# Kernel tuning notes

Measured on AMD Instinct MI355X. Metric: run time of the kernel, lower is better.

The kernel has to match this reference:

```python
import jax, jax.numpy as jnp
import numpy as np

GRID = (128, 128, 16)
VSIZE = 0.5  # voxel_size, pc_range = 0
B, V, N, K, C = 2, 100000, 8192, 8, 64
EPS = 1e-5
OFFSETS = [(dx, dy, dz) for dx in (-1, 0, 1) for dy in (-1, 0, 1) for dz in (-1, 0, 1)]


def setup_inputs() -> dict:
    key = jax.random.key(0)
    ks = jax.random.split(key, 8)
    world = jnp.array([GRID[0] * VSIZE, GRID[1] * VSIZE, GRID[2] * VSIZE], jnp.float32)
    keypoints = jax.random.uniform(ks[0], (B, N, K, 3), jnp.float32) * world
    query_feature = jax.random.normal(ks[1], (B, N, C), jnp.float32)
    voxel_feature = jax.random.normal(ks[2], (B, V, C), jnp.float32)
    # unique voxel coords per batch (hash-map / sparse-tensor semantics)
    cells = GRID[0] * GRID[1] * GRID[2]
    perm = jax.vmap(lambda k: jax.random.permutation(k, cells)[:V])(jax.random.split(ks[3], B))
    x = perm // (GRID[1] * GRID[2])
    rem = perm % (GRID[1] * GRID[2])
    voxel_coords = jnp.stack([x, rem // GRID[2], rem % GRID[2]], -1).astype(jnp.int32)
    W1 = jax.random.normal(ks[4], (27, C, C), jnp.float32) * 0.05
    W2 = jax.random.normal(ks[5], (27, C, C), jnp.float32) * 0.05
    proj_W = jax.random.normal(ks[6], (C, C), jnp.float32) / np.sqrt(C).astype(np.float32)
    proj_b = jnp.zeros((C,), jnp.float32)
    return dict(keypoints=keypoints, query_feature=query_feature,
                voxel_feature=voxel_feature, voxel_coords=voxel_coords,
                W1=W1, bn1_gamma=jnp.ones((C,), jnp.float32), bn1_beta=jnp.zeros((C,), jnp.float32),
                W2=W2, bn2_gamma=jnp.ones((C,), jnp.float32), bn2_beta=jnp.zeros((C,), jnp.float32),
                proj_W=proj_W, proj_b=proj_b)


def _subm_conv(feats, grid, cb, cxyz, W):
    # feats: (M, C); grid: (B, X, Y, Z) int32 flat row index or -1; W: (27, Cin, Cout)
    out = jnp.zeros((feats.shape[0], W.shape[-1]), feats.dtype)
    for k, (dx, dy, dz) in enumerate(OFFSETS):
        nx, ny, nz = cxyz[:, 0] + dx, cxyz[:, 1] + dy, cxyz[:, 2] + dz
        valid = (nx >= 0) & (nx < GRID[0]) & (ny >= 0) & (ny < GRID[1]) & (nz >= 0) & (nz < GRID[2])
        nidx = grid[cb, jnp.clip(nx, 0, GRID[0] - 1), jnp.clip(ny, 0, GRID[1] - 1), jnp.clip(nz, 0, GRID[2] - 1)]
        nidx = jnp.where(valid, nidx, -1)
        nf = jnp.where((nidx >= 0)[:, None], feats[jnp.maximum(nidx, 0)], jnp.zeros((), feats.dtype))
        out = out + nf @ W[k]
    return out


def _bn_relu(x, gamma, beta):
    # BatchNorm1d in training mode: batch stats (biased var), then ReLU
    mu = x.mean(0)
    var = jnp.var(x, axis=0)
    return jax.nn.relu((x - mu) * jax.lax.rsqrt(var + EPS) * gamma + beta)


def reference(keypoints, query_feature, voxel_feature, voxel_coords,
              W1, bn1_gamma, bn1_beta, W2, bn2_gamma, bn2_beta, proj_W, proj_b):
    coords = voxel_coords.reshape(-1, 3).astype(jnp.int32)
    cb = jnp.repeat(jnp.arange(B, dtype=jnp.int32), V)
    # dense grid hash: cell -> flat voxel row, -1 if empty (replaces Python dict)
    grid = jnp.full((B,) + GRID, -1, jnp.int32)
    grid = grid.at[cb, coords[:, 0], coords[:, 1], coords[:, 2]].set(jnp.arange(B * V, dtype=jnp.int32))
    feats = voxel_feature.reshape(-1, C)
    feats = _bn_relu(_subm_conv(feats, grid, cb, coords, W1), bn1_gamma, bn1_beta)
    feats = _bn_relu(_subm_conv(feats, grid, cb, coords, W2), bn2_gamma, bn2_beta)
    # quantize keypoints (pc_range = 0, trunc == floor since coords >= 0)
    q = (keypoints / VSIZE).astype(jnp.int32)
    q = jnp.clip(q, 0, jnp.array(GRID, jnp.int32) - 1)  # (B, N, K, 3)
    bidx = jnp.arange(B, dtype=jnp.int32)[:, None, None]
    idx = grid[bidx, q[..., 0], q[..., 1], q[..., 2]]   # (B, N, K); -1 -> fallback row 0
    sampled = feats[jnp.maximum(idx, 0)]                 # (B, N, K, C)
    fused = (sampled.mean(2) + query_feature) @ proj_W.T + proj_b
    voxel_indices = jnp.concatenate(
        [jnp.broadcast_to(bidx[..., None], (B, N, K, 1)), q], axis=-1).reshape(-1, 4)
    return fused, voxel_indices
```

## Files before the change

### kernel.cpp

```cpp
#include <hip/hip_runtime.h>
#include <hip/hip_bf16.h>
#include <math.h>

#define GX 128
#define GY 128
#define GZ 16
#define CELLS (GX*GY*GZ)
#define NCELLT (NB*CELLS)
#define NB 2
#define NV 100000
#define NM (NB*NV)
#define NN 8192
#define NK 8
#define NC 64
#define EPSV 1e-5f
#define TM 256
#define NTILE 98
#define NBLK (8*NTILE)
#define NMT (NBLK*TM)
#define KPH 7

typedef __attribute__((ext_vector_type(8))) short short8;
typedef __attribute__((ext_vector_type(4))) float floatx4;

__device__ __forceinline__ float bf2f(unsigned short u) {
    unsigned int x = ((unsigned int)u) << 16;
    return __builtin_bit_cast(float, x);
}
__device__ __forceinline__ unsigned short f2bf(float f) {
    unsigned int u = __builtin_bit_cast(unsigned int, f);
    return (unsigned short)((u + 0x7fffu + ((u >> 16) & 1u)) >> 16);
}

__global__ void k_init(int* __restrict__ grid, float* __restrict__ stats,
                       unsigned short* __restrict__ featA) {
    int i = blockIdx.x * 256 + threadIdx.x;
    if (i < NCELLT) grid[i] = -1;
    else if (i < NCELLT + 512) stats[i - NCELLT] = 0.f;
    else if (i < NCELLT + 512 + 64) featA[(size_t)NM * 64 + (i - NCELLT - 512)] = 0;
}

__global__ void k_scatter(const int* __restrict__ coords, int* __restrict__ grid) {
    int gid = blockIdx.x * 256 + threadIdx.x;
    if (gid >= NM) return;
    int b = (gid >= NV) ? 1 : 0;
    int x = coords[gid * 3 + 0];
    int y = coords[gid * 3 + 1];
    int z = coords[gid * 3 + 2];
    grid[((b * GX + x) * GY + y) * GZ + z] = gid;
}

__global__ void k_count(const int* __restrict__ grid, int* __restrict__ bcnt) {
    __shared__ int wt[4];
    int t = threadIdx.x;
    int occ = (grid[blockIdx.x * 256 + t] >= 0) ? 1 : 0;
    int w = t >> 6;
    unsigned long long m = __ballot(occ);
    if ((t & 63) == 0) wt[w] = __popcll(m);
    __syncthreads();
    if (t == 0) bcnt[blockIdx.x] = wt[0] + wt[1] + wt[2] + wt[3];
}

__global__ void k_scan2048(const int* __restrict__ bcnt, int* __restrict__ boff) {
    __shared__ int s[256];
    int t = threadIdx.x;
    int v[8], sum = 0;
    #pragma unroll
    for (int j = 0; j < 8; ++j) {
        int x = bcnt[t * 8 + j];
        v[j] = sum;
        sum += x;
    }
    s[t] = sum;
    __syncthreads();
    for (int off = 1; off < 256; off <<= 1) {
        int x = (t >= off) ? s[t - off] : 0;
        __syncthreads();
        s[t] += x;
        __syncthreads();
    }
    int excl = s[t] - sum;
    #pragma unroll
    for (int j = 0; j < 8; ++j) boff[t * 8 + j] = excl + v[j];
}

__global__ void k_assign(const int* __restrict__ gold, const int* __restrict__ boff,
                         int* __restrict__ gnew, int* __restrict__ perm,
                         int* __restrict__ scell) {
    __shared__ int wt[4];
    int t = threadIdx.x;
    int cell = blockIdx.x * 256 + t;
    int old = gold[cell];
    int occ = (old >= 0) ? 1 : 0;
    int w = t >> 6, lane = t & 63;
    unsigned long long m = __ballot(occ);
    int lp = __popcll(m & ((1ULL << lane) - 1ULL));
    if (lane == 63) wt[w] = lp + occ;
    __syncthreads();
    int wbase = 0;
    #pragma unroll
    for (int j = 0; j < 4; ++j) if (j < w) wbase += wt[j];
    int nid = boff[blockIdx.x] + wbase + lp;
    if (occ) {
        gnew[cell] = nid;
        perm[nid] = old;
        scell[nid] = cell;
    } else {
        gnew[cell] = -1;
    }
}

__global__ void k_fb(const int* __restrict__ vcoords, const int* __restrict__ gnew,
                     int* __restrict__ fbp) {
    if (threadIdx.x == 0 && blockIdx.x == 0) {
        int cell = (vcoords[0] * GY + vcoords[1]) * GZ + vcoords[2];
        fbp[0] = gnew[cell];
    }
}

__global__ void k_nbr(const int* __restrict__ scell, const int* __restrict__ gnew,
                      int* __restrict__ nid) {
    int m = blockIdx.x * 256 + threadIdx.x;
    if (m >= NMT) return;
    int cell = (m < NM) ? scell[m] : -1;
    int x = 0, y = 0, z = 0;
    if (cell >= 0) { x = (cell >> 11) & 127; y = (cell >> 4) & 127; z = cell & 15; }
    #pragma unroll
    for (int k = 0; k < 28; ++k) {
        int ni = NM;
        if (k < 27 && cell >= 0) {
            int dx = k / 9 - 1, dy = (k / 3) % 3 - 1, dz = k % 3 - 1;
            int nx = x + dx, ny = y + dy, nz = z + dz;
            if (nx >= 0 && nx < GX && ny >= 0 && ny < GY && nz >= 0 && nz < GZ) {
                int g = gnew[cell + dx * (GY * GZ) + dy * GZ + dz];
                ni = (g < 0) ? NM : g;
            }
        }
        nid[(size_t)k * NMT + m] = ni;
    }
}

__global__ void k_wprep(const float* __restrict__ W1, const float* __restrict__ W2,
                        unsigned short* __restrict__ Wt1, unsigned short* __restrict__ Wt2) {
    int e = blockIdx.x * 256 + threadIdx.x;
    if (e >= 28 * 512) return;
    int lane = e & 63;
    int fr = (e >> 6) & 7;
    int k = e >> 9;
    int ct = fr >> 1, ks = fr & 1;
    int quad = lane >> 4, n16 = lane & 15;
    int co = ct * 16 + n16;
    #pragma unroll
    for (int j = 0; j < 8; ++j) {
        int ci = ks * 32 + quad * 8 + j;
        unsigned short w1 = 0, w2 = 0;
        if (k < 27) {
            w1 = f2bf(W1[(k << 12) + ci * 64 + co]);
            w2 = f2bf(W2[(k << 12) + ci * 64 + co]);
        }
        Wt1[(size_t)e * 8 + j] = w1;
        Wt2[(size_t)e * 8 + j] = w2;
    }
}

__global__ void k_tobf16s(const float* __restrict__ in, const int* __restrict__ perm,
                          unsigned short* __restrict__ out) {
    int i = blockIdx.x * 256 + threadIdx.x;
    if (i >= NM * 8) return;
    int mrow = i >> 3, part = i & 7;
    int src = perm[mrow];
    const float4* s = (const float4*)(in + (size_t)src * 64 + part * 8);
    float4 a = s[0], b = s[1];
    ushort4 lo, hi;
    lo.x = f2bf(a.x); lo.y = f2bf(a.y); lo.z = f2bf(a.z); lo.w = f2bf(a.w);
    hi.x = f2bf(b.x); hi.y = f2bf(b.y); hi.z = f2bf(b.z); hi.w = f2bf(b.w);
    ushort4* d = (ushort4*)(out + (size_t)mrow * 64 + part * 8);
    d[0] = lo; d[1] = hi;
}

__global__ __launch_bounds__(256, 2) void k_conv(
    const unsigned short* __restrict__ feats, const int* __restrict__ nid,
    const unsigned short* __restrict__ Wt,
    unsigned short* __restrict__ out, float* __restrict__ gsum, float* __restrict__ gsq)
{
    __shared__ unsigned short s_b[KPH * 4096];

    int tid = threadIdx.x;
    int bid = blockIdx.x;
    int tile = (bid & 7) * NTILE + (bid >> 3);
    int m0 = tile * TM;

    int w = tid >> 6, lane = tid & 63;
    int quad = lane >> 4, n16 = lane & 15;
    const unsigned short* fq = feats + quad * 8;
    const int* nbase = nid + m0 + w * 64 + n16;

    short8 afr[3][8];

    auto issueA = [&](const int* nr, short8* af) {
        #pragma unroll
        for (int rt = 0; rt < 4; ++rt) {
            const unsigned short* r0 = fq + (size_t)nr[rt] * 64;
            af[rt * 2 + 0] = *(const short8*)(r0);
            af[rt * 2 + 1] = *(const short8*)(r0 + 32);
        }
    };

    floatx4 acc[4][4];
    #pragma unroll
    for (int rt = 0; rt < 4; ++rt)
        #pragma unroll
        for (int ct = 0; ct < 4; ++ct)
            acc[rt][ct] = (floatx4){0.f, 0.f, 0.f, 0.f};

    const uint4* wt4 = (const uint4*)Wt;

    for (int ph = 0; ph < 4; ++ph) {
        int k0 = ph * KPH;
        __syncthreads();

        uint4 breg[KPH * 2];
        #pragma unroll
        for (int i = 0; i < KPH * 2; ++i)
            breg[i] = wt4[(size_t)k0 * 512 + i * 256 + tid];

        int nidr[KPH][4];
        #pragma unroll
        for (int j = 0; j < KPH; ++j)
            #pragma unroll
            for (int rt = 0; rt < 4; ++rt)
                nidr[j][rt] = nbase[(size_t)(k0 + j) * NMT + rt * 16];

        #pragma unroll
        for (int i = 0; i < KPH * 2; ++i)
            ((uint4*)s_b)[i * 256 + tid] = breg[i];

        issueA(nidr[0], afr[0]);
        issueA(nidr[1], afr[1]);
        __syncthreads();

        #pragma unroll
        for (int j = 0; j < KPH; ++j) {
            if (j + 2 < KPH) issueA(nidr[j + 2], afr[(j + 2) % 3]);
            __builtin_amdgcn_sched_barrier(0);

            const unsigned short* bb = s_b + j * 4096;
            short8 bfr[8];
            #pragma unroll
            for (int fr = 0; fr < 8; ++fr)
                bfr[fr] = *(const short8*)(bb + fr * 512 + lane * 8);

            const short8* ac = afr[j % 3];
            #pragma unroll
            for (int ks = 0; ks < 2; ++ks)
                #pragma unroll
                for (int rt = 0; rt < 4; ++rt)
                    #pragma unroll
                    for (int ct = 0; ct < 4; ++ct)
                        acc[rt][ct] = __builtin_amdgcn_mfma_f32_16x16x32_bf16(
                            ac[rt * 2 + ks], bfr[ct * 2 + ks], acc[rt][ct], 0, 0, 0);
            __builtin_amdgcn_sched_barrier(0);
        }
    }

    #pragma unroll
    for (int rt = 0; rt < 4; ++rt) {
        int rbase = m0 + w * 64 + rt * 16 + quad * 4;
        #pragma unroll
        for (int rg = 0; rg < 4; ++rg) {
            int m = rbase + rg;
            if (m < NM) {
                #pragma unroll
                for (int ct = 0; ct < 4; ++ct)
                    out[(size_t)m * 64 + ct * 16 + n16] = f2bf(acc[rt][ct][rg]);
            }
        }
    }

    float ps[4], pq[4];
    #pragma unroll
    for (int ct = 0; ct < 4; ++ct) { ps[ct] = 0.f; pq[ct] = 0.f; }
    #pragma unroll
    for (int rt = 0; rt < 4; ++rt)
        #pragma unroll
        for (int ct = 0; ct < 4; ++ct)
            #pragma unroll
            for (int rg = 0; rg < 4; ++rg) {
                float v = acc[rt][ct][rg];
                ps[ct] += v;
                pq[ct] += v * v;
            }
    #pragma unroll
    for (int ct = 0; ct < 4; ++ct) {
        ps[ct] += __shfl_xor(ps[ct], 16);
        ps[ct] += __shfl_xor(ps[ct], 32);
        pq[ct] += __shfl_xor(pq[ct], 16);
        pq[ct] += __shfl_xor(pq[ct], 32);
    }
    __syncthreads();
    float* red = (float*)s_b;
    if (lane < 16) {
        #pragma unroll
        for (int ct = 0; ct < 4; ++ct) {
            red[w * 64 + ct * 16 + n16]       = ps[ct];
            red[256 + w * 64 + ct * 16 + n16] = pq[ct];
        }
    }
    __syncthreads();
    if (tid < 64) {
        float ts = 0.f, tq = 0.f;
        #pragma unroll
        for (int ww = 0; ww < 4; ++ww) {
            ts += red[ww * 64 + tid];
            tq += red[256 + ww * 64 + tid];
        }
        atomicAdd(gsum + tid, ts);
        atomicAdd(gsq + tid, tq);
    }
}

__global__ void k_bncoef(const float* __restrict__ gsum, const float* __restrict__ gsq,
                         const float* __restrict__ gamma, const float* __restrict__ beta,
                         float* __restrict__ coef) {
    int c = threadIdx.x;
    if (c >= 64) return;
    float mu = gsum[c] / (float)NM;
    float var = gsq[c] / (float)NM - mu * mu;
    float scale = gamma[c] / sqrtf(var + EPSV);
    coef[c] = scale;
    coef[64 + c] = beta[c] - mu * scale;
}

__global__ void k_bnapply(const unsigned short* __restrict__ in, const float* __restrict__ coef,
                          unsigned short* __restrict__ out) {
    int i = blockIdx.x * 256 + threadIdx.x;
    if (i >= NM * 8) return;
    int c8 = (i & 7) * 8;
    uint4 v = ((const uint4*)in)[i];
    unsigned int vv[4] = {v.x, v.y, v.z, v.w};
    unsigned int oo[4];
    #pragma unroll
    for (int j = 0; j < 4; ++j) {
        int c = c8 + j * 2;
        float lo = bf2f((unsigned short)(vv[j] & 0xffffu));
        float hi = bf2f((unsigned short)(vv[j] >> 16));
        lo = fmaxf(lo * coef[c]     + coef[64 + c],     0.f);
        hi = fmaxf(hi * coef[c + 1] + coef[64 + c + 1], 0.f);
        oo[j] = (unsigned int)f2bf(lo) | ((unsigned int)f2bf(hi) << 16);
    }
    uint4 o = {oo[0], oo[1], oo[2], oo[3]};
    ((uint4*)out)[i] = o;
}

__global__ __launch_bounds__(256) void k_sample(
    const float* __restrict__ kp, const float* __restrict__ query,
    const unsigned short* __restrict__ conv2, const float* __restrict__ coef2,
    const int* __restrict__ grid, const int* __restrict__ fbp,
    const float* __restrict__ projW, const float* __restrict__ projB,
    float* __restrict__ out_fused, float* __restrict__ out_vi)
{
    __shared__ float s_pw[64 * 65];
    __shared__ float s_mean[4][64];
    __shared__ int   s_idx[4][8];

    int tid = threadIdx.x;
    for (int e = tid; e < 4096; e += 256) {
        int co = e >> 6, c = e & 63;
        s_pw[co * 65 + c] = projW[e];
    }

    int w = tid >> 6, lane = tid & 63;
    int row = blockIdx.x * 4 + w;
    int b = row >> 13;
    float sc = coef2[lane];
    float sh = coef2[64 + lane];
    int fb = fbp[0];
    __syncthreads();

    if (lane < 8) {
        int kk = lane;
        const float* kpp = kp + ((size_t)row * 8 + kk) * 3;
        int qx = min(max((int)(kpp[0] * 2.0f), 0), GX - 1);
        int qy = min(max((int)(kpp[1] * 2.0f), 0), GY - 1);
        int qz = min(max((int)(kpp[2] * 2.0f), 0), GZ - 1);
        s_idx[w][kk] = grid[((b * GX + qx) * GY + qy) * GZ + qz];
        float4 vi = make_float4((float)b, (float)qx, (float)qy, (float)qz);
        *(float4*)(out_vi + ((size_t)row * 8 + kk) * 4) = vi;
    }
    __syncthreads();

    float acc = 0.f;
    #pragma unroll
    for (int kk = 0; kk < 8; ++kk) {
        int gi = s_idx[w][kk];
        gi = gi < 0 ? fb : gi;
        float v = bf2f(conv2[(size_t)gi * 64 + lane]);
        acc += fmaxf(v * sc + sh, 0.f);
    }
    float mean = acc * 0.125f + query[(size_t)row * 64 + lane];
    s_mean[w][lane] = mean;
    __syncthreads();

    float f = projB[lane];
    const float* pwr = s_pw + lane * 65;
    const float* mv = s_mean[w];
    #pragma unroll 8
    for (int c = 0; c < 64; ++c) f += mv[c] * pwr[c];
    out_fused[(size_t)row * 64 + lane] = f;
}

extern "C" void kernel_launch(void* const* d_in, const int* in_sizes, int n_in,
                              void* d_out, int out_size, void* d_ws, size_t ws_size,
                              hipStream_t stream) {
    const float* keypoints = (const float*)d_in[0];
    const float* query     = (const float*)d_in[1];
    const float* vfeat     = (const float*)d_in[2];
    const int*   vcoords   = (const int*)d_in[3];
    const float* W1        = (const float*)d_in[4];
    const float* g1        = (const float*)d_in[5];
    const float* b1        = (const float*)d_in[6];
    const float* W2        = (const float*)d_in[7];
    const float* g2        = (const float*)d_in[8];
    const float* b2        = (const float*)d_in[9];
    const float* pW        = (const float*)d_in[10];
    const float* pb        = (const float*)d_in[11];

    char* ws = (char*)d_ws;
    int*            gold  = (int*)ws;
    int*            gnew  = (int*)(ws + 2097152);
    float*          stats = (float*)(ws + 4194304);
    int*            fbp   = (int*)(ws + 4196352);
    int*            bcnt  = (int*)(ws + 4196608);
    int*            boff  = (int*)(ws + 4204800);
    int*            perm  = (int*)(ws + 4212992);
    int*            scell = (int*)(ws + 5012992);
    unsigned short* Wt1   = (unsigned short*)(ws + 5812992);
    unsigned short* Wt2   = (unsigned short*)(ws + 6042368);
    unsigned short* featA = (unsigned short*)(ws + 6271744);
    int*            nidt  = (int*)(ws + 31872000);
    unsigned short* convo = (unsigned short*)(ws + 54350848);

    float* sum1 = stats,       *sq1 = stats + 64,  *coef1 = stats + 128;
    float* sum2 = stats + 256, *sq2 = stats + 320, *coef2 = stats + 384;

    int initN = NCELLT + 512 + 64;
    k_init<<<(initN + 255) / 256, 256, 0, stream>>>(gold, stats, featA);
    k_scatter<<<(NM + 255) / 256, 256, 0, stream>>>(vcoords, gold);

    k_count<<<NCELLT / 256, 256, 0, stream>>>(gold, bcnt);
    k_scan2048<<<1, 256, 0, stream>>>(bcnt, boff);
    k_assign<<<NCELLT / 256, 256, 0, stream>>>(gold, boff, gnew, perm, scell);
    k_fb<<<1, 64, 0, stream>>>(vcoords, gnew, fbp);
    k_nbr<<<NMT / 256, 256, 0, stream>>>(scell, gnew, nidt);

    k_wprep<<<(28 * 512 + 255) / 256, 256, 0, stream>>>(W1, W2, Wt1, Wt2);
    k_tobf16s<<<(NM * 8 + 255) / 256, 256, 0, stream>>>(vfeat, perm, featA);

    k_conv<<<NBLK, 256, 0, stream>>>(featA, nidt, Wt1, convo, sum1, sq1);
    k_bncoef<<<1, 64, 0, stream>>>(sum1, sq1, g1, b1, coef1);
    k_bnapply<<<(NM * 8 + 255) / 256, 256, 0, stream>>>(convo, coef1, featA);

    k_conv<<<NBLK, 256, 0, stream>>>(featA, nidt, Wt2, convo, sum2, sq2);
    k_bncoef<<<1, 64, 0, stream>>>(sum2, sq2, g2, b2, coef2);

    float* out_fused = (float*)d_out;
    float* out_vi = out_fused + (size_t)NB * NN * NC;
    k_sample<<<(NB * NN) / 4, 256, 0, stream>>>(keypoints, query, convo, coef2, gnew, fbp,
                                                pW, pb, out_fused, out_vi);
}
```

Before: 343.8 us.

## Fuse small prep kernels, fold BN coef into consumers, retile conv to 128 rows

Merges the fallback lookup into the neighbor kernel and the weight prep into the feature bf16 conversion kernel. The BN coefficient kernels are dropped by recomputing the coefficients inside the apply and sample kernels. This removes several launches at the cost of some redundant per-thread arithmetic. The conv kernel moves to 128-row tiles with 4 offsets per phase and 3 blocks per CU, double-buffering the neighbor indices across phases to raise occupancy and overlap the gathers.

```diff
diff --git a/kernel.cpp b/kernel.cpp
--- a/kernel.cpp
+++ b/kernel.cpp
@@ -14,11 +14,11 @@
 #define NK 8
 #define NC 64
 #define EPSV 1e-5f
-#define TM 256
-#define NTILE 98
+#define TM 128
+#define NTILE 196
 #define NBLK (8*NTILE)
 #define NMT (NBLK*TM)
-#define KPH 7
+#define KPH 4
 
 typedef __attribute__((ext_vector_type(8))) short short8;
 typedef __attribute__((ext_vector_type(4))) float floatx4;
@@ -110,16 +110,13 @@
     }
 }
 
-__global__ void k_fb(const int* __restrict__ vcoords, const int* __restrict__ gnew,
-                     int* __restrict__ fbp) {
-    if (threadIdx.x == 0 && blockIdx.x == 0) {
-        int cell = (vcoords[0] * GY + vcoords[1]) * GZ + vcoords[2];
-        fbp[0] = gnew[cell];
-    }
-}
-
 __global__ void k_nbr(const int* __restrict__ scell, const int* __restrict__ gnew,
-                      int* __restrict__ nid) {
+                      const int* __restrict__ vcoords,
+                      int* __restrict__ nid, int* __restrict__ fbp) {
+    if (blockIdx.x == 0 && threadIdx.x == 0) {
+        int cell0 = (vcoords[0] * GY + vcoords[1]) * GZ + vcoords[2];
+        fbp[0] = gnew[cell0];
+    }
     int m = blockIdx.x * 256 + threadIdx.x;
     if (m >= NMT) return;
     int cell = (m < NM) ? scell[m] : -1;
@@ -140,45 +137,46 @@
     }
 }
 
-__global__ void k_wprep(const float* __restrict__ W1, const float* __restrict__ W2,
-                        unsigned short* __restrict__ Wt1, unsigned short* __restrict__ Wt2) {
-    int e = blockIdx.x * 256 + threadIdx.x;
-    if (e >= 28 * 512) return;
-    int lane = e & 63;
-    int fr = (e >> 6) & 7;
-    int k = e >> 9;
-    int ct = fr >> 1, ks = fr & 1;
-    int quad = lane >> 4, n16 = lane & 15;
-    int co = ct * 16 + n16;
-    #pragma unroll
-    for (int j = 0; j < 8; ++j) {
-        int ci = ks * 32 + quad * 8 + j;
-        unsigned short w1 = 0, w2 = 0;
-        if (k < 27) {
-            w1 = f2bf(W1[(k << 12) + ci * 64 + co]);
-            w2 = f2bf(W2[(k << 12) + ci * 64 + co]);
-        }
-        Wt1[(size_t)e * 8 + j] = w1;
-        Wt2[(size_t)e * 8 + j] = w2;
-    }
-}
-
-__global__ void k_tobf16s(const float* __restrict__ in, const int* __restrict__ perm,
-                          unsigned short* __restrict__ out) {
-    int i = blockIdx.x * 256 + threadIdx.x;
-    if (i >= NM * 8) return;
-    int mrow = i >> 3, part = i & 7;
-    int src = perm[mrow];
-    const float4* s = (const float4*)(in + (size_t)src * 64 + part * 8);
-    float4 a = s[0], b = s[1];
-    ushort4 lo, hi;
-    lo.x = f2bf(a.x); lo.y = f2bf(a.y); lo.z = f2bf(a.z); lo.w = f2bf(a.w);
-    hi.x = f2bf(b.x); hi.y = f2bf(b.y); hi.z = f2bf(b.z); hi.w = f2bf(b.w);
-    ushort4* d = (ushort4*)(out + (size_t)mrow * 64 + part * 8);
-    d[0] = lo; d[1] = hi;
-}
-
-__global__ __launch_bounds__(256, 2) void k_conv(
+__global__ void k_prep(const float* __restrict__ W1, const float* __restrict__ W2,
+                       const float* __restrict__ vfeat, const int* __restrict__ perm,
+                       unsigned short* __restrict__ Wt1, unsigned short* __restrict__ Wt2,
+                       unsigned short* __restrict__ featA) {
+    int bid = blockIdx.x;
+    if (bid < 56) {
+        int e = bid * 256 + threadIdx.x;
+        int lane = e & 63;
+        int fr = (e >> 6) & 7;
+        int k = e >> 9;
+        int ct = fr >> 1, ks = fr & 1;
+        int quad = lane >> 4, n16 = lane & 15;
+        int co = ct * 16 + n16;
+        #pragma unroll
+        for (int j = 0; j < 8; ++j) {
+            int ci = ks * 32 + quad * 8 + j;
+            unsigned short w1 = 0, w2 = 0;
+            if (k < 27) {
+                w1 = f2bf(W1[(k << 12) + ci * 64 + co]);
+                w2 = f2bf(W2[(k << 12) + ci * 64 + co]);
+            }
+            Wt1[(size_t)e * 8 + j] = w1;
+            Wt2[(size_t)e * 8 + j] = w2;
+        }
+    } else {
+        int i = (bid - 56) * 256 + threadIdx.x;
+        if (i >= NM * 8) return;
+        int mrow = i >> 3, part = i & 7;
+        int src = perm[mrow];
+        const float4* s = (const float4*)(vfeat + (size_t)src * 64 + part * 8);
+        float4 a = s[0], b = s[1];
+        ushort4 lo, hi;
+        lo.x = f2bf(a.x); lo.y = f2bf(a.y); lo.z = f2bf(a.z); lo.w = f2bf(a.w);
+        hi.x = f2bf(b.x); hi.y = f2bf(b.y); hi.z = f2bf(b.z); hi.w = f2bf(b.w);
+        ushort4* d = (ushort4*)(featA + (size_t)mrow * 64 + part * 8);
+        d[0] = lo; d[1] = hi;
+    }
+}
+
+__global__ __launch_bounds__(256, 3) void k_conv(
     const unsigned short* __restrict__ feats, const int* __restrict__ nid,
     const unsigned short* __restrict__ Wt,
     unsigned short* __restrict__ out, float* __restrict__ gsum, float* __restrict__ gsq)
@@ -193,55 +191,56 @@
     int w = tid >> 6, lane = tid & 63;
     int quad = lane >> 4, n16 = lane & 15;
     const unsigned short* fq = feats + quad * 8;
-    const int* nbase = nid + m0 + w * 64 + n16;
-
-    short8 afr[3][8];
+    const int* nbase = nid + m0 + w * 32 + n16;
+
+    short8 afr[3][4];
+    int nidr[2][KPH][2];
 
     auto issueA = [&](const int* nr, short8* af) {
         #pragma unroll
-        for (int rt = 0; rt < 4; ++rt) {
+        for (int rt = 0; rt < 2; ++rt) {
             const unsigned short* r0 = fq + (size_t)nr[rt] * 64;
             af[rt * 2 + 0] = *(const short8*)(r0);
             af[rt * 2 + 1] = *(const short8*)(r0 + 32);
         }
     };
 
-    floatx4 acc[4][4];
-    #pragma unroll
-    for (int rt = 0; rt < 4; ++rt)
+    floatx4 acc[2][4];
+    #pragma unroll
+    for (int rt = 0; rt < 2; ++rt)
         #pragma unroll
         for (int ct = 0; ct < 4; ++ct)
             acc[rt][ct] = (floatx4){0.f, 0.f, 0.f, 0.f};
 
     const uint4* wt4 = (const uint4*)Wt;
 
-    for (int ph = 0; ph < 4; ++ph) {
+    #pragma unroll
+    for (int j = 0; j < KPH; ++j) {
+        nidr[0][j][0] = nbase[(size_t)j * NMT];
+        nidr[0][j][1] = nbase[(size_t)j * NMT + 16];
+    }
+
+    for (int ph = 0; ph < 7; ++ph) {
         int k0 = ph * KPH;
+        int cur = ph & 1;
         __syncthreads();
-
-        uint4 breg[KPH * 2];
         #pragma unroll
         for (int i = 0; i < KPH * 2; ++i)
-            breg[i] = wt4[(size_t)k0 * 512 + i * 256 + tid];
-
-        int nidr[KPH][4];
-        #pragma unroll
-        for (int j = 0; j < KPH; ++j)
+            ((uint4*)s_b)[i * 256 + tid] = wt4[(size_t)k0 * 512 + i * 256 + tid];
+        if (ph < 6) {
             #pragma unroll
-            for (int rt = 0; rt < 4; ++rt)
-                nidr[j][rt] = nbase[(size_t)(k0 + j) * NMT + rt * 16];
-
-        #pragma unroll
-        for (int i = 0; i < KPH * 2; ++i)
-            ((uint4*)s_b)[i * 256 + tid] = breg[i];
-
-        issueA(nidr[0], afr[0]);
-        issueA(nidr[1], afr[1]);
+            for (int j = 0; j < KPH; ++j) {
+                nidr[cur ^ 1][j][0] = nbase[(size_t)(k0 + KPH + j) * NMT];
+                nidr[cur ^ 1][j][1] = nbase[(size_t)(k0 + KPH + j) * NMT + 16];
+            }
+        }
+        issueA(nidr[cur][0], afr[0]);
+        issueA(nidr[cur][1], afr[1]);
         __syncthreads();
 
         #pragma unroll
         for (int j = 0; j < KPH; ++j) {
-            if (j + 2 < KPH) issueA(nidr[j + 2], afr[(j + 2) % 3]);
+            if (j + 2 < KPH) issueA(nidr[cur][j + 2], afr[(j + 2) % 3]);
             __builtin_amdgcn_sched_barrier(0);
 
             const unsigned short* bb = s_b + j * 4096;
@@ -254,7 +253,7 @@
             #pragma unroll
             for (int ks = 0; ks < 2; ++ks)
                 #pragma unroll
-                for (int rt = 0; rt < 4; ++rt)
+                for (int rt = 0; rt < 2; ++rt)
                     #pragma unroll
                     for (int ct = 0; ct < 4; ++ct)
                         acc[rt][ct] = __builtin_amdgcn_mfma_f32_16x16x32_bf16(
@@ -264,8 +263,8 @@
     }
 
     #pragma unroll
-    for (int rt = 0; rt < 4; ++rt) {
-        int rbase = m0 + w * 64 + rt * 16 + quad * 4;
+    for (int rt = 0; rt < 2; ++rt) {
+        int rbase = m0 + w * 32 + rt * 16 + quad * 4;
         #pragma unroll
         for (int rg = 0; rg < 4; ++rg) {
             int m = rbase + rg;
@@ -281,7 +280,7 @@
     #pragma unroll
     for (int ct = 0; ct < 4; ++ct) { ps[ct] = 0.f; pq[ct] = 0.f; }
     #pragma unroll
-    for (int rt = 0; rt < 4; ++rt)
+    for (int rt = 0; rt < 2; ++rt)
         #pragma unroll
         for (int ct = 0; ct < 4; ++ct)
             #pragma unroll
@@ -319,33 +318,32 @@
     }
 }
 
-__global__ void k_bncoef(const float* __restrict__ gsum, const float* __restrict__ gsq,
-                         const float* __restrict__ gamma, const float* __restrict__ beta,
-                         float* __restrict__ coef) {
-    int c = threadIdx.x;
-    if (c >= 64) return;
-    float mu = gsum[c] / (float)NM;
-    float var = gsq[c] / (float)NM - mu * mu;
-    float scale = gamma[c] / sqrtf(var + EPSV);
-    coef[c] = scale;
-    coef[64 + c] = beta[c] - mu * scale;
-}
-
-__global__ void k_bnapply(const unsigned short* __restrict__ in, const float* __restrict__ coef,
+__global__ void k_bnapply(const unsigned short* __restrict__ in,
+                          const float* __restrict__ gsum, const float* __restrict__ gsq,
+                          const float* __restrict__ gamma, const float* __restrict__ beta,
                           unsigned short* __restrict__ out) {
     int i = blockIdx.x * 256 + threadIdx.x;
     if (i >= NM * 8) return;
     int c8 = (i & 7) * 8;
+    float scv[8], shv[8];
+    #pragma unroll
+    for (int jj = 0; jj < 8; ++jj) {
+        int c = c8 + jj;
+        float mu = gsum[c] * (1.f / NM);
+        float var = gsq[c] * (1.f / NM) - mu * mu;
+        float s = gamma[c] * rsqrtf(var + EPSV);
+        scv[jj] = s;
+        shv[jj] = beta[c] - mu * s;
+    }
     uint4 v = ((const uint4*)in)[i];
     unsigned int vv[4] = {v.x, v.y, v.z, v.w};
     unsigned int oo[4];
     #pragma unroll
     for (int j = 0; j < 4; ++j) {
-        int c = c8 + j * 2;
         float lo = bf2f((unsigned short)(vv[j] & 0xffffu));
         float hi = bf2f((unsigned short)(vv[j] >> 16));
-        lo = fmaxf(lo * coef[c]     + coef[64 + c],     0.f);
-        hi = fmaxf(hi * coef[c + 1] + coef[64 + c + 1], 0.f);
+        lo = fmaxf(lo * scv[j * 2]     + shv[j * 2],     0.f);
+        hi = fmaxf(hi * scv[j * 2 + 1] + shv[j * 2 + 1], 0.f);
         oo[j] = (unsigned int)f2bf(lo) | ((unsigned int)f2bf(hi) << 16);
     }
     uint4 o = {oo[0], oo[1], oo[2], oo[3]};
@@ -354,7 +352,9 @@
 
 __global__ __launch_bounds__(256) void k_sample(
     const float* __restrict__ kp, const float* __restrict__ query,
-    const unsigned short* __restrict__ conv2, const float* __restrict__ coef2,
+    const unsigned short* __restrict__ conv2,
+    const float* __restrict__ gsum2, const float* __restrict__ gsq2,
+    const float* __restrict__ g2, const float* __restrict__ b2,
     const int* __restrict__ grid, const int* __restrict__ fbp,
     const float* __restrict__ projW, const float* __restrict__ projB,
     float* __restrict__ out_fused, float* __restrict__ out_vi)
@@ -372,8 +372,10 @@
     int w = tid >> 6, lane = tid & 63;
     int row = blockIdx.x * 4 + w;
     int b = row >> 13;
-    float sc = coef2[lane];
-    float sh = coef2[64 + lane];
+    float mu = gsum2[lane] * (1.f / NM);
+    float var = gsq2[lane] * (1.f / NM) - mu * mu;
+    float sc = g2[lane] * rsqrtf(var + EPSV);
+    float sh = b2[lane] - mu * sc;
     int fb = fbp[0];
     __syncthreads();
 
@@ -440,8 +442,8 @@
     int*            nidt  = (int*)(ws + 31872000);
     unsigned short* convo = (unsigned short*)(ws + 54350848);
 
-    float* sum1 = stats,       *sq1 = stats + 64,  *coef1 = stats + 128;
-    float* sum2 = stats + 256, *sq2 = stats + 320, *coef2 = stats + 384;
+    float* sum1 = stats,       *sq1 = stats + 64;
+    float* sum2 = stats + 256, *sq2 = stats + 320;
 
     int initN = NCELLT + 512 + 64;
     k_init<<<(initN + 255) / 256, 256, 0, stream>>>(gold, stats, featA);
@@ -450,21 +452,18 @@
     k_count<<<NCELLT / 256, 256, 0, stream>>>(gold, bcnt);
     k_scan2048<<<1, 256, 0, stream>>>(bcnt, boff);
     k_assign<<<NCELLT / 256, 256, 0, stream>>>(gold, boff, gnew, perm, scell);
-    k_fb<<<1, 64, 0, stream>>>(vcoords, gnew, fbp);
-    k_nbr<<<NMT / 256, 256, 0, stream>>>(scell, gnew, nidt);
-
-    k_wprep<<<(28 * 512 + 255) / 256, 256, 0, stream>>>(W1, W2, Wt1, Wt2);
-    k_tobf16s<<<(NM * 8 + 255) / 256, 256, 0, stream>>>(vfeat, perm, featA);
+    k_nbr<<<NMT / 256, 256, 0, stream>>>(scell, gnew, vcoords, nidt, fbp);
+
+    k_prep<<<56 + (NM * 8 + 255) / 256, 256, 0, stream>>>(W1, W2, vfeat, perm,
+                                                          Wt1, Wt2, featA);
 
     k_conv<<<NBLK, 256, 0, stream>>>(featA, nidt, Wt1, convo, sum1, sq1);
-    k_bncoef<<<1, 64, 0, stream>>>(sum1, sq1, g1, b1, coef1);
-    k_bnapply<<<(NM * 8 + 255) / 256, 256, 0, stream>>>(convo, coef1, featA);
+    k_bnapply<<<(NM * 8 + 255) / 256, 256, 0, stream>>>(convo, sum1, sq1, g1, b1, featA);
 
     k_conv<<<NBLK, 256, 0, stream>>>(featA, nidt, Wt2, convo, sum2, sq2);
-    k_bncoef<<<1, 64, 0, stream>>>(sum2, sq2, g2, b2, coef2);
 
     float* out_fused = (float*)d_out;
     float* out_vi = out_fused + (size_t)NB * NN * NC;
-    k_sample<<<(NB * NN) / 4, 256, 0, stream>>>(keypoints, query, convo, coef2, gnew, fbp,
-                                                pW, pb, out_fused, out_vi);
-}
+    k_sample<<<(NB * NN) / 4, 256, 0, stream>>>(keypoints, query, convo, sum2, sq2, g2, b2,
+                                                gnew, fbp, pW, pb, out_fused, out_vi);
+}
```

Result: faster. 325.0 us (-5.5%).
